# Kernel optimization log

Hardware: AMD Instinct MI355X
Metric: run time of the kernel (lower is better)

## Reference

```python
import jax, jax.numpy as jnp
import numpy as np

B, L, DIM, H = 1, 2048, 1536, 12
HD = DIM // H  # 128
SCALE = HD ** -0.5


def quantize_dequant_int8(t):
    # per-tensor symmetric int8 quantize then float dequantize (same math as torch ref)
    s = jnp.max(jnp.abs(t)) / 127.0
    q = jnp.clip(jnp.round(t / s), -128.0, 127.0)
    return q * s


def setup_inputs() -> dict:
    key = jax.random.key(0)
    ks = jax.random.split(key, 6)
    std = DIM ** -0.5
    return {
        "x": jax.random.normal(ks[0], (B, L, DIM), jnp.float32),
        "Wq": jax.random.normal(ks[1], (DIM, DIM), jnp.float32) * std,
        "Wk": jax.random.normal(ks[2], (DIM, DIM), jnp.float32) * std,
        "Wv": jax.random.normal(ks[3], (DIM, DIM), jnp.float32) * std,
        "Wo": jax.random.normal(ks[4], (DIM, DIM), jnp.float32) * std,
        "bo": jax.random.normal(ks[5], (DIM,), jnp.float32) * 0.01,
    }


def reference(x, Wq, Wk, Wv, Wo, bo):
    b, l, c = x.shape
    # QKV projections (torch Linear: x @ W^T), reshape to [B,H,L,HD]
    q = (x @ Wq.T).reshape(b, l, H, HD).transpose(0, 2, 1, 3)
    k = (x @ Wk.T).reshape(b, l, H, HD).transpose(0, 2, 1, 3)
    v = (x @ Wv.T).reshape(b, l, H, HD).transpose(0, 2, 1, 3)
    # sage-style quantize/dequant around both matmuls
    qd = quantize_dequant_int8(q)
    kd = quantize_dequant_int8(k)
    scores = jnp.einsum('bhqd,bhkd->bhqk', qd, kd) * SCALE
    probs = jax.nn.softmax(scores, axis=-1)
    pd = quantize_dequant_int8(probs)
    vd = quantize_dequant_int8(v)
    out = jnp.einsum('bhqk,bhkd->bhqd', pd, vd)  # [B,H,L,HD]
    out = out.transpose(0, 2, 1, 3).reshape(b, l, c)
    return out @ Wo.T + bo
```

## Files before the change

kernel.cpp:

```cpp
#include <hip/hip_runtime.h>
#include <stdint.h>

#define SEQ 2048
#define DIM 1536
#define NH  12
#define HD  128
#define SCALEF 0.08838834764831845f
#define LDP 40

typedef __attribute__((ext_vector_type(8))) short short8;
typedef __attribute__((ext_vector_type(4))) float floatx4;

#define MFMA16(a, b, c) __builtin_amdgcn_mfma_f32_16x16x32_bf16((a), (b), (c), 0, 0, 0)

__device__ __forceinline__ void async_cp16(const void* g, void* l) {
  __builtin_amdgcn_global_load_lds(
      (__attribute__((address_space(1))) unsigned int*)(g),
      (__attribute__((address_space(3))) unsigned int*)(l), 16, 0, 0);
}

__device__ __forceinline__ unsigned short f2bf(float f) {
  unsigned int u = __float_as_uint(f);
  u = (u + 0x7fff + ((u >> 16) & 1)) >> 16;
  return (unsigned short)u;
}

__device__ __forceinline__ void split8v(const float* x, short8& h, short8& l) {
#pragma unroll
  for (int e = 0; e < 8; e++) {
    unsigned int u = __float_as_uint(x[e]);
    h[e] = (short)(u >> 16);
    float r = x[e] - __uint_as_float(u & 0xFFFF0000u);
    l[e] = (short)f2bf(r);
  }
}
__device__ __forceinline__ void split8(const float* g, short8& h, short8& l) {
  float4 f0 = *(const float4*)g, f1 = *(const float4*)(g + 4);
  float x[8] = {f0.x, f0.y, f0.z, f0.w, f1.x, f1.y, f1.z, f1.w};
  split8v(x, h, l);
}

__global__ __launch_bounds__(256) void k_fill(float* __restrict__ out, int n,
                                              float val) {
  int i = blockIdx.x * 256 + threadIdx.x;
  if (i < n) out[i] = val;
}

__global__ __launch_bounds__(256) void k_gemm_qkv(
    const float* __restrict__ X, const float* __restrict__ Wq,
    const float* __restrict__ Wk, const float* __restrict__ Wv,
    float* __restrict__ qf, float* __restrict__ kf, float* __restrict__ vf,
    unsigned int* __restrict__ scal) {
  __shared__ __align__(16) unsigned short Ah[128 * LDP], Al[128 * LDP];
  __shared__ __align__(16) unsigned short Bh[128 * LDP], Bl[128 * LDP];
  int tid = threadIdx.x, z = blockIdx.z;
  const float* W = (z == 0) ? Wq : (z == 1) ? Wk : Wv;
  float* C = (z == 0) ? qf : (z == 1) ? kf : vf;
  int n0 = blockIdx.x * 128, m0 = blockIdx.y * 128;
  int lane = tid & 63, w = tid >> 6;
  int wr = w >> 1, wc = w & 1, lm = lane & 15, q = lane >> 4;

  floatx4 acc[4][4];
#pragma unroll
  for (int i = 0; i < 4; i++)
#pragma unroll
    for (int j = 0; j < 4; j++) acc[i][j] = (floatx4){0.f, 0.f, 0.f, 0.f};

  int rowA = tid >> 2, c8 = tid & 3;
  for (int k0 = 0; k0 < DIM; k0 += 32) {
    __syncthreads();
#pragma unroll
    for (int i = 0; i < 2; i++) {
      int r = i * 64 + rowA;
      short8 h, l;
      split8(X + (size_t)(m0 + r) * DIM + k0 + c8 * 8, h, l);
      *(short8*)(Ah + r * LDP + c8 * 8) = h;
      *(short8*)(Al + r * LDP + c8 * 8) = l;
      split8(W + (size_t)(n0 + r) * DIM + k0 + c8 * 8, h, l);
      *(short8*)(Bh + r * LDP + c8 * 8) = h;
      *(short8*)(Bl + r * LDP + c8 * 8) = l;
    }
    __syncthreads();
    short8 ah[4], al[4], bh[4], bl[4];
#pragma unroll
    for (int i = 0; i < 4; i++) {
      int r = wr * 64 + i * 16 + lm;
      ah[i] = *(const short8*)(Ah + r * LDP + q * 8);
      al[i] = *(const short8*)(Al + r * LDP + q * 8);
    }
#pragma unroll
    for (int j = 0; j < 4; j++) {
      int r = wc * 64 + j * 16 + lm;
      bh[j] = *(const short8*)(Bh + r * LDP + q * 8);
      bl[j] = *(const short8*)(Bl + r * LDP + q * 8);
    }
#pragma unroll
    for (int i = 0; i < 4; i++)
#pragma unroll
      for (int j = 0; j < 4; j++) {
        acc[i][j] = MFMA16(ah[i], bh[j], acc[i][j]);
        acc[i][j] = MFMA16(ah[i], bl[j], acc[i][j]);
        acc[i][j] = MFMA16(al[i], bh[j], acc[i][j]);
      }
  }
  float am = 0.f;
#pragma unroll
  for (int i = 0; i < 4; i++) {
    int row = m0 + wr * 64 + i * 16 + q * 4;
#pragma unroll
    for (int j = 0; j < 4; j++) {
      int col = n0 + wc * 64 + j * 16 + lm;
#pragma unroll
      for (int r = 0; r < 4; r++) {
        float v = acc[i][j][r];
        C[(size_t)(row + r) * DIM + col] = v;
        am = fmaxf(am, fabsf(v));
      }
    }
  }
#pragma unroll
  for (int mk = 32; mk >= 1; mk >>= 1) am = fmaxf(am, __shfl_xor(am, mk, 64));
  if (lane == 0) atomicMax(&scal[z], __float_as_uint(am));
}

__global__ __launch_bounds__(256) void k_quant_vT(
    const float* __restrict__ vf, const unsigned int* __restrict__ scal,
    unsigned short* __restrict__ nvT) {
  __shared__ float T[64 * 65];
  int h = blockIdx.z, d0 = blockIdx.y * 64, k0 = blockIdx.x * 64;
  float s = __uint_as_float(scal[2]) / 127.f;
  int t = threadIdx.x;
#pragma unroll
  for (int i = 0; i < 16; i++) {
    int idx = i * 256 + t;
    int r = idx >> 6, c = idx & 63;
    float v = vf[(size_t)(k0 + r) * DIM + h * HD + d0 + c];
    T[r * 65 + c] = fminf(fmaxf(rintf(v / s), -128.f), 127.f);
  }
  __syncthreads();
#pragma unroll
  for (int i = 0; i < 16; i++) {
    int idx = i * 256 + t;
    int d = idx >> 6, r = idx & 63;
    nvT[(size_t)(h * HD + d0 + d) * SEQ + k0 + r] = f2bf(T[r * 65 + d]);
  }
}

__global__ __launch_bounds__(256) void k_quant_qk(
    const float* __restrict__ qf, const float* __restrict__ kf,
    const unsigned int* __restrict__ scal,
    unsigned short* __restrict__ nq, unsigned short* __restrict__ nk) {
  int z = blockIdx.y;
  const float* src = z ? kf : qf;
  unsigned short* dst = z ? nk : nq;
  float s = __uint_as_float(scal[z]) / 127.f;
  size_t i = ((size_t)blockIdx.x * 256 + threadIdx.x) * 4;
  float4 v = *(const float4*)(src + i);
  ushort4 o;
  o.x = f2bf(fminf(fmaxf(rintf(v.x / s), -128.f), 127.f));
  o.y = f2bf(fminf(fmaxf(rintf(v.y / s), -128.f), 127.f));
  o.z = f2bf(fminf(fmaxf(rintf(v.z / s), -128.f), 127.f));
  o.w = f2bf(fminf(fmaxf(rintf(v.w / s), -128.f), 127.f));
  *(ushort4*)(dst + i) = o;
}

__global__ __launch_bounds__(256) void k_stats(
    const unsigned short* __restrict__ nq, const unsigned short* __restrict__ nk,
    const unsigned int* __restrict__ scal, float* __restrict__ pstats) {
  __shared__ unsigned short Ks[32 * 128];
  int h = blockIdx.y, tid = threadIdx.x, lane = tid & 63, w = tid >> 6;
  int lm = lane & 15, q = lane >> 4;
  int qb = blockIdx.x & 15, chunk = blockIdx.x >> 4;
  int mb = qb * 128 + w * 32;
  int kbase = chunk * 256;
  float f = (__uint_as_float(scal[0]) / 127.f) *
            (__uint_as_float(scal[1]) / 127.f) * SCALEF;

  short8 aq[2][4];
#pragma unroll
  for (int mi = 0; mi < 2; mi++) {
    const unsigned short* qb_p =
        nq + (size_t)(mb + mi * 16 + lm) * DIM + h * HD + q * 8;
#pragma unroll
    for (int cc = 0; cc < 4; cc++) aq[mi][cc] = *(const short8*)(qb_p + cc * 32);
  }

  float m[2][4], zz[2][4];
#pragma unroll
  for (int mi = 0; mi < 2; mi++)
#pragma unroll
    for (int r = 0; r < 4; r++) { m[mi][r] = -3.0e38f; zz[mi][r] = 0.f; }

  for (int kt = kbase; kt < kbase + 256; kt += 32) {
    __syncthreads();
#pragma unroll
    for (int i = 0; i < 2; i++) {
      int ch = i * 256 + tid;
      int krow = ch >> 4;
      int gcol = (ch & 15) ^ (krow & 7);
      async_cp16(nk + (size_t)(kt + krow) * DIM + h * HD + gcol * 8,
                 Ks + ch * 8);
    }
    __syncthreads();
    short8 bk[2][4];
#pragma unroll
    for (int st = 0; st < 2; st++)
#pragma unroll
      for (int cc = 0; cc < 4; cc++) {
        int phys = (cc * 4 + q) ^ (lm & 7);
        bk[st][cc] = *(const short8*)(Ks + (st * 16 + lm) * 128 + phys * 8);
      }
#pragma unroll
    for (int mi = 0; mi < 2; mi++) {
      floatx4 a0 = (floatx4){0.f, 0.f, 0.f, 0.f};
      floatx4 a1 = (floatx4){0.f, 0.f, 0.f, 0.f};
#pragma unroll
      for (int cc = 0; cc < 4; cc++) {
        a0 = MFMA16(aq[mi][cc], bk[0][cc], a0);
        a1 = MFMA16(aq[mi][cc], bk[1][cc], a1);
      }
#pragma unroll
      for (int r = 0; r < 4; r++) {
        float s0 = a0[r] * f, s1 = a1[r] * f;
        float nm = fmaxf(m[mi][r], fmaxf(s0, s1));
        zz[mi][r] = zz[mi][r] * expf(m[mi][r] - nm) + expf(s0 - nm) +
                    expf(s1 - nm);
        m[mi][r] = nm;
      }
    }
  }
#pragma unroll
  for (int mk = 1; mk < 16; mk <<= 1)
#pragma unroll
    for (int mi = 0; mi < 2; mi++)
#pragma unroll
      for (int r = 0; r < 4; r++) {
        float om = __shfl_xor(m[mi][r], mk, 64);
        float oz = __shfl_xor(zz[mi][r], mk, 64);
        float nm = fmaxf(m[mi][r], om);
        zz[mi][r] = zz[mi][r] * expf(m[mi][r] - nm) + oz * expf(om - nm);
        m[mi][r] = nm;
      }
  if (lm == 0) {
#pragma unroll
    for (int mi = 0; mi < 2; mi++)
#pragma unroll
      for (int r = 0; r < 4; r++) {
        int row = mb + mi * 16 + q * 4 + r;
        float* p = pstats + (((size_t)h * SEQ + row) * 8 + chunk) * 2;
        p[0] = m[mi][r];
        p[1] = zz[mi][r];
      }
  }
}

__global__ __launch_bounds__(256) void k_merge(
    const float* __restrict__ pstats, float* __restrict__ stats,
    unsigned int* __restrict__ minZ) {
  int idx = blockIdx.x * 256 + threadIdx.x;
  const float* p = pstats + (size_t)idx * 16;
  float M = -3.0e38f;
#pragma unroll
  for (int c = 0; c < 8; c++) M = fmaxf(M, p[c * 2]);
  float Z = 0.f;
#pragma unroll
  for (int c = 0; c < 8; c++) Z += p[c * 2 + 1] * expf(p[c * 2] - M);
  stats[(size_t)idx * 2] = M;
  stats[(size_t)idx * 2 + 1] = Z;
  atomicMin(minZ, __float_as_uint(Z));
}

__global__ __launch_bounds__(256) void k_attn(
    const unsigned short* __restrict__ nq, const unsigned short* __restrict__ nk,
    const unsigned short* __restrict__ nvT,
    const unsigned int* __restrict__ scal, const unsigned int* __restrict__ minZ,
    const float* __restrict__ stats, float* __restrict__ attn0,
    float* __restrict__ attn1) {
  __shared__ unsigned short Ks[32 * 128];
  __shared__ unsigned short Vs[128 * 32];
  __shared__ unsigned short Pl[4][2][16 * 40];
  int h = blockIdx.y, tid = threadIdx.x, lane = tid & 63, w = tid >> 6;
  int lm = lane & 15, q = lane >> 4;
  int qb = blockIdx.x & 15, chunk = blockIdx.x >> 4;
  int mb = qb * 128 + w * 32;
  float* attn = chunk ? attn1 : attn0;
  float sv = __uint_as_float(scal[2]) / 127.f;
  float f = (__uint_as_float(scal[0]) / 127.f) *
            (__uint_as_float(scal[1]) / 127.f) * SCALEF;
  float sp = (1.f / __uint_as_float(*minZ)) / 127.f;
  float inv_sp = 1.f / sp;

  short8 aq[2][4];
#pragma unroll
  for (int mi = 0; mi < 2; mi++) {
    const unsigned short* qb_p =
        nq + (size_t)(mb + mi * 16 + lm) * DIM + h * HD + q * 8;
#pragma unroll
    for (int cc = 0; cc < 4; cc++) aq[mi][cc] = *(const short8*)(qb_p + cc * 32);
  }
  float M[2][4], invZ[2][4];
#pragma unroll
  for (int mi = 0; mi < 2; mi++)
#pragma unroll
    for (int r = 0; r < 4; r++) {
      int row = mb + mi * 16 + q * 4 + r;
      M[mi][r] = stats[((size_t)h * SEQ + row) * 2];
      invZ[mi][r] = 1.f / stats[((size_t)h * SEQ + row) * 2 + 1];
    }
  floatx4 accO[2][8];
#pragma unroll
  for (int mi = 0; mi < 2; mi++)
#pragma unroll
    for (int j = 0; j < 8; j++) accO[mi][j] = (floatx4){0.f, 0.f, 0.f, 0.f};

  int kbase = chunk * 1024;
  for (int kt = kbase; kt < kbase + 1024; kt += 32) {
    __syncthreads();
#pragma unroll
    for (int i = 0; i < 2; i++) {
      int ch = i * 256 + tid;
      int krow = ch >> 4;
      int gcol = (ch & 15) ^ (krow & 7);
      async_cp16(nk + (size_t)(kt + krow) * DIM + h * HD + gcol * 8,
                 Ks + ch * 8);
      int d = ch >> 2;
      int vcol = (ch & 3) ^ ((d >> 1) & 3);
      async_cp16(nvT + (size_t)(h * HD + d) * SEQ + kt + vcol * 8,
                 Vs + ch * 8);
    }
    __syncthreads();
    short8 bk[2][4];
#pragma unroll
    for (int st = 0; st < 2; st++)
#pragma unroll
      for (int cc = 0; cc < 4; cc++) {
        int phys = (cc * 4 + q) ^ (lm & 7);
        bk[st][cc] = *(const short8*)(Ks + (st * 16 + lm) * 128 + phys * 8);
      }
#pragma unroll
    for (int mi = 0; mi < 2; mi++)
#pragma unroll
      for (int st = 0; st < 2; st++) {
        floatx4 acc = (floatx4){0.f, 0.f, 0.f, 0.f};
#pragma unroll
        for (int cc = 0; cc < 4; cc++) acc = MFMA16(aq[mi][cc], bk[st][cc], acc);
#pragma unroll
        for (int r = 0; r < 4; r++) {
          float t = expf(acc[r] * f - M[mi][r]);
          float n = rintf(t * invZ[mi][r] * inv_sp);
          n = fminf(n, 127.f);
          Pl[w][mi][(q * 4 + r) * 40 + st * 16 + lm] = f2bf(n);
        }
      }
    __syncthreads();
    short8 ap[2];
#pragma unroll
    for (int mi = 0; mi < 2; mi++)
      ap[mi] = *(const short8*)(&Pl[w][mi][lm * 40 + q * 8]);
#pragma unroll
    for (int j = 0; j < 8; j++) {
      int d = j * 16 + lm;
      int vphys = q ^ ((d >> 1) & 3);
      short8 bv = *(const short8*)(Vs + d * 32 + vphys * 8);
#pragma unroll
      for (int mi = 0; mi < 2; mi++) accO[mi][j] = MFMA16(ap[mi], bv, accO[mi][j]);
    }
  }
  float osc = sp * sv;
#pragma unroll
  for (int mi = 0; mi < 2; mi++)
#pragma unroll
    for (int j = 0; j < 8; j++)
#pragma unroll
      for (int r = 0; r < 4; r++)
        attn[(size_t)(mb + mi * 16 + q * 4 + r) * DIM + h * HD + j * 16 + lm] =
            accO[mi][j][r] * osc;
}

__global__ __launch_bounds__(256) void k_gemm_out(
    const float* __restrict__ A0, const float* __restrict__ A1,
    const float* __restrict__ Wo, const float* __restrict__ bo,
    float* __restrict__ out) {
  __shared__ __align__(16) unsigned short Ah[128 * LDP], Al[128 * LDP];
  __shared__ __align__(16) unsigned short Bh[128 * LDP], Bl[128 * LDP];
  int tid = threadIdx.x;
  int n0 = blockIdx.x * 128, m0 = blockIdx.y * 128;
  int lane = tid & 63, w = tid >> 6;
  int wr = w >> 1, wc = w & 1, lm = lane & 15, q = lane >> 4;

  floatx4 acc[4][4];
#pragma unroll
  for (int i = 0; i < 4; i++)
#pragma unroll
    for (int j = 0; j < 4; j++) acc[i][j] = (floatx4){0.f, 0.f, 0.f, 0.f};

  int rowA = tid >> 2, c8 = tid & 3;
  for (int k0 = 0; k0 < DIM; k0 += 32) {
    __syncthreads();
#pragma unroll
    for (int i = 0; i < 2; i++) {
      int r = i * 64 + rowA;
      size_t off = (size_t)(m0 + r) * DIM + k0 + c8 * 8;
      float4 x0 = *(const float4*)(A0 + off), x1 = *(const float4*)(A0 + off + 4);
      float4 y0 = *(const float4*)(A1 + off), y1 = *(const float4*)(A1 + off + 4);
      float xs[8] = {x0.x + y0.x, x0.y + y0.y, x0.z + y0.z, x0.w + y0.w,
                     x1.x + y1.x, x1.y + y1.y, x1.z + y1.z, x1.w + y1.w};
      short8 h, l;
      split8v(xs, h, l);
      *(short8*)(Ah + r * LDP + c8 * 8) = h;
      *(short8*)(Al + r * LDP + c8 * 8) = l;
      split8(Wo + (size_t)(n0 + r) * DIM + k0 + c8 * 8, h, l);
      *(short8*)(Bh + r * LDP + c8 * 8) = h;
      *(short8*)(Bl + r * LDP + c8 * 8) = l;
    }
    __syncthreads();
    short8 ah[4], al[4], bh[4], bl[4];
#pragma unroll
    for (int i = 0; i < 4; i++) {
      int r = wr * 64 + i * 16 + lm;
      ah[i] = *(const short8*)(Ah + r * LDP + q * 8);
      al[i] = *(const short8*)(Al + r * LDP + q * 8);
    }
#pragma unroll
    for (int j = 0; j < 4; j++) {
      int r = wc * 64 + j * 16 + lm;
      bh[j] = *(const short8*)(Bh + r * LDP + q * 8);
      bl[j] = *(const short8*)(Bl + r * LDP + q * 8);
    }
#pragma unroll
    for (int i = 0; i < 4; i++)
#pragma unroll
      for (int j = 0; j < 4; j++) {
        acc[i][j] = MFMA16(ah[i], bh[j], acc[i][j]);
        acc[i][j] = MFMA16(ah[i], bl[j], acc[i][j]);
        acc[i][j] = MFMA16(al[i], bh[j], acc[i][j]);
      }
  }
#pragma unroll
  for (int j = 0; j < 4; j++) {
    int col = n0 + wc * 64 + j * 16 + lm;
    float bias = bo[col];
#pragma unroll
    for (int i = 0; i < 4; i++) {
      int row = m0 + wr * 64 + i * 16 + q * 4;
#pragma unroll
      for (int r = 0; r < 4; r++)
        out[(size_t)(row + r) * DIM + col] = acc[i][j][r] + bias;
    }
  }
}

extern "C" void kernel_launch(void* const* d_in, const int* in_sizes, int n_in,
                              void* d_out, int out_size, void* d_ws, size_t ws_size,
                              hipStream_t stream) {
  float* out = (float*)d_out;
  bool sizes_ok = (n_in >= 6) && in_sizes && in_sizes[0] == SEQ * DIM &&
                  in_sizes[1] == DIM * DIM && in_sizes[2] == DIM * DIM &&
                  in_sizes[3] == DIM * DIM && in_sizes[4] == DIM * DIM &&
                  in_sizes[5] == DIM && out_size == SEQ * DIM;
  if (!sizes_ok) {
    k_fill<<<(out_size + 255) / 256, 256, 0, stream>>>(out, out_size, 1.0f);
    return;
  }
  if (ws_size < 50528272) {
    k_fill<<<(out_size + 255) / 256, 256, 0, stream>>>(out, out_size, 2.0f);
    return;
  }

  const float* x  = (const float*)d_in[0];
  const float* Wq = (const float*)d_in[1];
  const float* Wk = (const float*)d_in[2];
  const float* Wv = (const float*)d_in[3];
  const float* Wo = (const float*)d_in[4];
  const float* bo = (const float*)d_in[5];
  char* ws = (char*)d_ws;

  float* qf = (float*)(ws);
  float* kf = (float*)(ws + 12582912);
  float* vf = (float*)(ws + 25165824);
  unsigned short* nq  = (unsigned short*)(ws + 25165824);
  float* pstats = (float*)(ws + 31457280);
  unsigned short* nvT = (unsigned short*)(ws + 37748736);
  unsigned short* nk  = (unsigned short*)(ws + 44040192);
  float* attn0 = qf;
  float* attn1 = kf;
  float* stats = (float*)(ws + 50331648);
  unsigned int* scal = (unsigned int*)(ws + 50528256);

  hipMemsetAsync(scal, 0, 12, stream);
  hipMemsetAsync(scal + 3, 0x7f, 4, stream);

  k_gemm_qkv<<<dim3(DIM / 128, SEQ / 128, 3), 256, 0, stream>>>(
      x, Wq, Wk, Wv, qf, kf, vf, scal);
  k_quant_vT<<<dim3(SEQ / 64, HD / 64, NH), 256, 0, stream>>>(vf, scal, nvT);
  k_quant_qk<<<dim3((SEQ * DIM) / 1024, 2), 256, 0, stream>>>(qf, kf, scal, nq, nk);
  k_stats<<<dim3(8 * 16, NH), 256, 0, stream>>>(nq, nk, scal, pstats);
  k_merge<<<dim3(NH * SEQ / 256), 256, 0, stream>>>(pstats, stats, scal + 3);
  k_attn<<<dim3(2 * 16, NH), 256, 0, stream>>>(nq, nk, nvT, scal, scal + 3,
                                               stats, attn0, attn1);
  k_gemm_out<<<dim3(DIM / 128, SEQ / 128), 256, 0, stream>>>(attn0, attn1, Wo,
                                                             bo, out);
}
```

Before: 531.7 us.

## Double-buffer LDS tiles with register prefetch in QKV and output GEMMs

The QKV and output projection GEMMs now use two LDS buffers. The next K-slice's global loads are issued into registers before the current slice's MFMAs, then split into bf16 hi/lo and stored into the other buffer afterwards. This hides global-load latency behind compute and removes one of the two barriers per iteration. In exchange it doubles LDS use per block (about 80KB), which may lower occupancy, and adds register pressure from the prefetched float4 values.

```diff
diff --git a/kernel.cpp b/kernel.cpp
--- a/kernel.cpp
+++ b/kernel.cpp
@@ -51,8 +51,8 @@
     const float* __restrict__ Wk, const float* __restrict__ Wv,
     float* __restrict__ qf, float* __restrict__ kf, float* __restrict__ vf,
     unsigned int* __restrict__ scal) {
-  __shared__ __align__(16) unsigned short Ah[128 * LDP], Al[128 * LDP];
-  __shared__ __align__(16) unsigned short Bh[128 * LDP], Bl[128 * LDP];
+  __shared__ __align__(16) unsigned short Ah[2][128 * LDP], Al[2][128 * LDP];
+  __shared__ __align__(16) unsigned short Bh[2][128 * LDP], Bl[2][128 * LDP];
   int tid = threadIdx.x, z = blockIdx.z;
   const float* W = (z == 0) ? Wq : (z == 1) ? Wk : Wv;
   float* C = (z == 0) ? qf : (z == 1) ? kf : vf;
@@ -67,32 +67,59 @@
     for (int j = 0; j < 4; j++) acc[i][j] = (floatx4){0.f, 0.f, 0.f, 0.f};
 
   int rowA = tid >> 2, c8 = tid & 3;
-  for (int k0 = 0; k0 < DIM; k0 += 32) {
-    __syncthreads();
-#pragma unroll
-    for (int i = 0; i < 2; i++) {
-      int r = i * 64 + rowA;
-      short8 h, l;
-      split8(X + (size_t)(m0 + r) * DIM + k0 + c8 * 8, h, l);
-      *(short8*)(Ah + r * LDP + c8 * 8) = h;
-      *(short8*)(Al + r * LDP + c8 * 8) = l;
-      split8(W + (size_t)(n0 + r) * DIM + k0 + c8 * 8, h, l);
-      *(short8*)(Bh + r * LDP + c8 * 8) = h;
-      *(short8*)(Bl + r * LDP + c8 * 8) = l;
-    }
-    __syncthreads();
+  const float* pA0 = X + (size_t)(m0 + rowA) * DIM + c8 * 8;
+  const float* pA1 = pA0 + (size_t)64 * DIM;
+  const float* pB0 = W + (size_t)(n0 + rowA) * DIM + c8 * 8;
+  const float* pB1 = pB0 + (size_t)64 * DIM;
+
+  {
+    short8 h, l;
+    split8(pA0, h, l);
+    *(short8*)(&Ah[0][0] + rowA * LDP + c8 * 8) = h;
+    *(short8*)(&Al[0][0] + rowA * LDP + c8 * 8) = l;
+    split8(pA1, h, l);
+    *(short8*)(&Ah[0][0] + (64 + rowA) * LDP + c8 * 8) = h;
+    *(short8*)(&Al[0][0] + (64 + rowA) * LDP + c8 * 8) = l;
+    split8(pB0, h, l);
+    *(short8*)(&Bh[0][0] + rowA * LDP + c8 * 8) = h;
+    *(short8*)(&Bl[0][0] + rowA * LDP + c8 * 8) = l;
+    split8(pB1, h, l);
+    *(short8*)(&Bh[0][0] + (64 + rowA) * LDP + c8 * 8) = h;
+    *(short8*)(&Bl[0][0] + (64 + rowA) * LDP + c8 * 8) = l;
+  }
+  __syncthreads();
+
+  int cur = 0;
+  for (int it = 0; it < DIM / 32; ++it) {
+    int kn = it * 32 + 32;
+    bool more = kn < DIM;
+    float4 a00, a01, a10, a11, b00, b01, b10, b11;
+    if (more) {
+      a00 = *(const float4*)(pA0 + kn);
+      a01 = *(const float4*)(pA0 + kn + 4);
+      a10 = *(const float4*)(pA1 + kn);
+      a11 = *(const float4*)(pA1 + kn + 4);
+      b00 = *(const float4*)(pB0 + kn);
+      b01 = *(const float4*)(pB0 + kn + 4);
+      b10 = *(const float4*)(pB1 + kn);
+      b11 = *(const float4*)(pB1 + kn + 4);
+    }
+    const unsigned short* AhC = &Ah[cur][0];
+    const unsigned short* AlC = &Al[cur][0];
+    const unsigned short* BhC = &Bh[cur][0];
+    const unsigned short* BlC = &Bl[cur][0];
     short8 ah[4], al[4], bh[4], bl[4];
 #pragma unroll
     for (int i = 0; i < 4; i++) {
       int r = wr * 64 + i * 16 + lm;
-      ah[i] = *(const short8*)(Ah + r * LDP + q * 8);
-      al[i] = *(const short8*)(Al + r * LDP + q * 8);
+      ah[i] = *(const short8*)(AhC + r * LDP + q * 8);
+      al[i] = *(const short8*)(AlC + r * LDP + q * 8);
     }
 #pragma unroll
     for (int j = 0; j < 4; j++) {
       int r = wc * 64 + j * 16 + lm;
-      bh[j] = *(const short8*)(Bh + r * LDP + q * 8);
-      bl[j] = *(const short8*)(Bl + r * LDP + q * 8);
+      bh[j] = *(const short8*)(BhC + r * LDP + q * 8);
+      bl[j] = *(const short8*)(BlC + r * LDP + q * 8);
     }
 #pragma unroll
     for (int i = 0; i < 4; i++)
@@ -102,6 +129,39 @@
         acc[i][j] = MFMA16(ah[i], bl[j], acc[i][j]);
         acc[i][j] = MFMA16(al[i], bh[j], acc[i][j]);
       }
+    if (more) {
+      unsigned short* AhN = &Ah[cur ^ 1][0];
+      unsigned short* AlN = &Al[cur ^ 1][0];
+      unsigned short* BhN = &Bh[cur ^ 1][0];
+      unsigned short* BlN = &Bl[cur ^ 1][0];
+      short8 h, l;
+      {
+        float xs[8] = {a00.x, a00.y, a00.z, a00.w, a01.x, a01.y, a01.z, a01.w};
+        split8v(xs, h, l);
+        *(short8*)(AhN + rowA * LDP + c8 * 8) = h;
+        *(short8*)(AlN + rowA * LDP + c8 * 8) = l;
+      }
+      {
+        float xs[8] = {a10.x, a10.y, a10.z, a10.w, a11.x, a11.y, a11.z, a11.w};
+        split8v(xs, h, l);
+        *(short8*)(AhN + (64 + rowA) * LDP + c8 * 8) = h;
+        *(short8*)(AlN + (64 + rowA) * LDP + c8 * 8) = l;
+      }
+      {
+        float xs[8] = {b00.x, b00.y, b00.z, b00.w, b01.x, b01.y, b01.z, b01.w};
+        split8v(xs, h, l);
+        *(short8*)(BhN + rowA * LDP + c8 * 8) = h;
+        *(short8*)(BlN + rowA * LDP + c8 * 8) = l;
+      }
+      {
+        float xs[8] = {b10.x, b10.y, b10.z, b10.w, b11.x, b11.y, b11.z, b11.w};
+        split8v(xs, h, l);
+        *(short8*)(BhN + (64 + rowA) * LDP + c8 * 8) = h;
+        *(short8*)(BlN + (64 + rowA) * LDP + c8 * 8) = l;
+      }
+      __syncthreads();
+    }
+    cur ^= 1;
   }
   float am = 0.f;
 #pragma unroll
@@ -381,8 +441,8 @@
     const float* __restrict__ A0, const float* __restrict__ A1,
     const float* __restrict__ Wo, const float* __restrict__ bo,
     float* __restrict__ out) {
-  __shared__ __align__(16) unsigned short Ah[128 * LDP], Al[128 * LDP];
-  __shared__ __align__(16) unsigned short Bh[128 * LDP], Bl[128 * LDP];
+  __shared__ __align__(16) unsigned short Ah[2][128 * LDP], Al[2][128 * LDP];
+  __shared__ __align__(16) unsigned short Bh[2][128 * LDP], Bl[2][128 * LDP];
   int tid = threadIdx.x;
   int n0 = blockIdx.x * 128, m0 = blockIdx.y * 128;
   int lane = tid & 63, w = tid >> 6;
@@ -395,37 +455,75 @@
     for (int j = 0; j < 4; j++) acc[i][j] = (floatx4){0.f, 0.f, 0.f, 0.f};
 
   int rowA = tid >> 2, c8 = tid & 3;
-  for (int k0 = 0; k0 < DIM; k0 += 32) {
-    __syncthreads();
-#pragma unroll
-    for (int i = 0; i < 2; i++) {
-      int r = i * 64 + rowA;
-      size_t off = (size_t)(m0 + r) * DIM + k0 + c8 * 8;
-      float4 x0 = *(const float4*)(A0 + off), x1 = *(const float4*)(A0 + off + 4);
-      float4 y0 = *(const float4*)(A1 + off), y1 = *(const float4*)(A1 + off + 4);
+  size_t offA0 = (size_t)(m0 + rowA) * DIM + c8 * 8;
+  size_t offA1 = offA0 + (size_t)64 * DIM;
+  const float* pB0 = Wo + (size_t)(n0 + rowA) * DIM + c8 * 8;
+  const float* pB1 = pB0 + (size_t)64 * DIM;
+
+  {
+    short8 h, l;
+    {
+      float4 x0 = *(const float4*)(A0 + offA0), x1 = *(const float4*)(A0 + offA0 + 4);
+      float4 y0 = *(const float4*)(A1 + offA0), y1 = *(const float4*)(A1 + offA0 + 4);
       float xs[8] = {x0.x + y0.x, x0.y + y0.y, x0.z + y0.z, x0.w + y0.w,
                      x1.x + y1.x, x1.y + y1.y, x1.z + y1.z, x1.w + y1.w};
-      short8 h, l;
       split8v(xs, h, l);
-      *(short8*)(Ah + r * LDP + c8 * 8) = h;
-      *(short8*)(Al + r * LDP + c8 * 8) = l;
-      split8(Wo + (size_t)(n0 + r) * DIM + k0 + c8 * 8, h, l);
-      *(short8*)(Bh + r * LDP + c8 * 8) = h;
-      *(short8*)(Bl + r * LDP + c8 * 8) = l;
-    }
-    __syncthreads();
+      *(short8*)(&Ah[0][0] + rowA * LDP + c8 * 8) = h;
+      *(short8*)(&Al[0][0] + rowA * LDP + c8 * 8) = l;
+    }
+    {
+      float4 x0 = *(const float4*)(A0 + offA1), x1 = *(const float4*)(A0 + offA1 + 4);
+      float4 y0 = *(const float4*)(A1 + offA1), y1 = *(const float4*)(A1 + offA1 + 4);
+      float xs[8] = {x0.x + y0.x, x0.y + y0.y, x0.z + y0.z, x0.w + y0.w,
+                     x1.x + y1.x, x1.y + y1.y, x1.z + y1.z, x1.w + y1.w};
+      split8v(xs, h, l);
+      *(short8*)(&Ah[0][0] + (64 + rowA) * LDP + c8 * 8) = h;
+      *(short8*)(&Al[0][0] + (64 + rowA) * LDP + c8 * 8) = l;
+    }
+    split8(pB0, h, l);
+    *(short8*)(&Bh[0][0] + rowA * LDP + c8 * 8) = h;
+    *(short8*)(&Bl[0][0] + rowA * LDP + c8 * 8) = l;
+    split8(pB1, h, l);
+    *(short8*)(&Bh[0][0] + (64 + rowA) * LDP + c8 * 8) = h;
+    *(short8*)(&Bl[0][0] + (64 + rowA) * LDP + c8 * 8) = l;
+  }
+  __syncthreads();
+
+  int cur = 0;
+  for (int it = 0; it < DIM / 32; ++it) {
+    int kn = it * 32 + 32;
+    bool more = kn < DIM;
+    float4 x00, x01, x10, x11, y00, y01, y10, y11, b00, b01, b10, b11;
+    if (more) {
+      x00 = *(const float4*)(A0 + offA0 + kn);
+      x01 = *(const float4*)(A0 + offA0 + kn + 4);
+      y00 = *(const float4*)(A1 + offA0 + kn);
+      y01 = *(const float4*)(A1 + offA0 + kn + 4);
+      x10 = *(const float4*)(A0 + offA1 + kn);
+      x11 = *(const float4*)(A0 + offA1 + kn + 4);
+      y10 = *(const float4*)(A1 + offA1 + kn);
+      y11 = *(const float4*)(A1 + offA1 + kn + 4);
+      b00 = *(const float4*)(pB0 + kn);
+      b01 = *(const float4*)(pB0 + kn + 4);
+      b10 = *(const float4*)(pB1 + kn);
+      b11 = *(const float4*)(pB1 + kn + 4);
+    }
+    const unsigned short* AhC = &Ah[cur][0];
+    const unsigned short* AlC = &Al[cur][0];
+    const unsigned short* BhC = &Bh[cur][0];
+    const unsigned short* BlC = &Bl[cur][0];
     short8 ah[4], al[4], bh[4], bl[4];
 #pragma unroll
     for (int i = 0; i < 4; i++) {
       int r = wr * 64 + i * 16 + lm;
-      ah[i] = *(const short8*)(Ah + r * LDP + q * 8);
-      al[i] = *(const short8*)(Al + r * LDP + q * 8);
+      ah[i] = *(const short8*)(AhC + r * LDP + q * 8);
+      al[i] = *(const short8*)(AlC + r * LDP + q * 8);
     }
 #pragma unroll
     for (int j = 0; j < 4; j++) {
       int r = wc * 64 + j * 16 + lm;
-      bh[j] = *(const short8*)(Bh + r * LDP + q * 8);
-      bl[j] = *(const short8*)(Bl + r * LDP + q * 8);
+      bh[j] = *(const short8*)(BhC + r * LDP + q * 8);
+      bl[j] = *(const short8*)(BlC + r * LDP + q * 8);
     }
 #pragma unroll
     for (int i = 0; i < 4; i++)
@@ -435,6 +533,41 @@
         acc[i][j] = MFMA16(ah[i], bl[j], acc[i][j]);
         acc[i][j] = MFMA16(al[i], bh[j], acc[i][j]);
       }
+    if (more) {
+      unsigned short* AhN = &Ah[cur ^ 1][0];
+      unsigned short* AlN = &Al[cur ^ 1][0];
+      unsigned short* BhN = &Bh[cur ^ 1][0];
+      unsigned short* BlN = &Bl[cur ^ 1][0];
+      short8 h, l;
+      {
+        float xs[8] = {x00.x + y00.x, x00.y + y00.y, x00.z + y00.z, x00.w + y00.w,
+                       x01.x + y01.x, x01.y + y01.y, x01.z + y01.z, x01.w + y01.w};
+        split8v(xs, h, l);
+        *(short8*)(AhN + rowA * LDP + c8 * 8) = h;
+        *(short8*)(AlN + rowA * LDP + c8 * 8) = l;
+      }
+      {
+        float xs[8] = {x10.x + y10.x, x10.y + y10.y, x10.z + y10.z, x10.w + y10.w,
+                       x11.x + y11.x, x11.y + y11.y, x11.z + y11.z, x11.w + y11.w};
+        split8v(xs, h, l);
+        *(short8*)(AhN + (64 + rowA) * LDP + c8 * 8) = h;
+        *(short8*)(AlN + (64 + rowA) * LDP + c8 * 8) = l;
+      }
+      {
+        float xs[8] = {b00.x, b00.y, b00.z, b00.w, b01.x, b01.y, b01.z, b01.w};
+        split8v(xs, h, l);
+        *(short8*)(BhN + rowA * LDP + c8 * 8) = h;
+        *(short8*)(BlN + rowA * LDP + c8 * 8) = l;
+      }
+      {
+        float xs[8] = {b10.x, b10.y, b10.z, b10.w, b11.x, b11.y, b11.z, b11.w};
+        split8v(xs, h, l);
+        *(short8*)(BhN + (64 + rowA) * LDP + c8 * 8) = h;
+        *(short8*)(BlN + (64 + rowA) * LDP + c8 * 8) = l;
+      }
+      __syncthreads();
+    }
+    cur ^= 1;
   }
 #pragma unroll
   for (int j = 0; j < 4; j++) {
```

Measured after the change: 536.8 us. About the same (+1.0%).

## Presplit GEMM activations to bf16 hi/lo and double-buffer tiles with async LDS loads

Applied to the files above, without the earlier changes.

Adds pre-pass kernels that split X and the summed attention output into bf16 high/low arrays once, instead of redoing the split inside every GEMM block. The QKV and output GEMMs now load A tiles straight into LDS with async global-to-LDS copies into a swizzled layout. Both LDS buffers are double-buffered so the next K-slice (async A, register-prefetched and split W) loads while the current one is in MFMAs, with one barrier per iteration. The cost is two extra kernel launches and extra global traffic for the split arrays, plus doubled shared memory per block, which can reduce occupancy.

```diff
diff --git a/kernel.cpp b/kernel.cpp
--- a/kernel.cpp
+++ b/kernel.cpp
@@ -46,13 +46,38 @@
   if (i < n) out[i] = val;
 }
 
+__global__ __launch_bounds__(256) void k_split_x(
+    const float* __restrict__ X, unsigned short* __restrict__ Xh,
+    unsigned short* __restrict__ Xl) {
+  size_t i = ((size_t)blockIdx.x * 256 + threadIdx.x) * 8;
+  short8 h, l;
+  split8(X + i, h, l);
+  *(short8*)(Xh + i) = h;
+  *(short8*)(Xl + i) = l;
+}
+
+__global__ __launch_bounds__(256) void k_split_o(
+    const float* __restrict__ A0, const float* __restrict__ A1,
+    unsigned short* __restrict__ Oh, unsigned short* __restrict__ Ol) {
+  size_t i = ((size_t)blockIdx.x * 256 + threadIdx.x) * 8;
+  float4 x0 = *(const float4*)(A0 + i), x1 = *(const float4*)(A0 + i + 4);
+  float4 y0 = *(const float4*)(A1 + i), y1 = *(const float4*)(A1 + i + 4);
+  float xs[8] = {x0.x + y0.x, x0.y + y0.y, x0.z + y0.z, x0.w + y0.w,
+                 x1.x + y1.x, x1.y + y1.y, x1.z + y1.z, x1.w + y1.w};
+  short8 h, l;
+  split8v(xs, h, l);
+  *(short8*)(Oh + i) = h;
+  *(short8*)(Ol + i) = l;
+}
+
 __global__ __launch_bounds__(256) void k_gemm_qkv(
-    const float* __restrict__ X, const float* __restrict__ Wq,
-    const float* __restrict__ Wk, const float* __restrict__ Wv,
-    float* __restrict__ qf, float* __restrict__ kf, float* __restrict__ vf,
+    const unsigned short* __restrict__ Xh, const unsigned short* __restrict__ Xl,
+    const float* __restrict__ Wq, const float* __restrict__ Wk,
+    const float* __restrict__ Wv, float* __restrict__ qf,
+    float* __restrict__ kf, float* __restrict__ vf,
     unsigned int* __restrict__ scal) {
-  __shared__ __align__(16) unsigned short Ah[128 * LDP], Al[128 * LDP];
-  __shared__ __align__(16) unsigned short Bh[128 * LDP], Bl[128 * LDP];
+  __shared__ __align__(16) unsigned short Ahs[2][128 * 32], Als[2][128 * 32];
+  __shared__ __align__(16) unsigned short Bh[2][128 * LDP], Bl[2][128 * LDP];
   int tid = threadIdx.x, z = blockIdx.z;
   const float* W = (z == 0) ? Wq : (z == 1) ? Wk : Wv;
   float* C = (z == 0) ? qf : (z == 1) ? kf : vf;
@@ -67,32 +92,93 @@
     for (int j = 0; j < 4; j++) acc[i][j] = (floatx4){0.f, 0.f, 0.f, 0.f};
 
   int rowA = tid >> 2, c8 = tid & 3;
-  for (int k0 = 0; k0 < DIM; k0 += 32) {
-    __syncthreads();
-#pragma unroll
-    for (int i = 0; i < 2; i++) {
-      int r = i * 64 + rowA;
-      short8 h, l;
-      split8(X + (size_t)(m0 + r) * DIM + k0 + c8 * 8, h, l);
-      *(short8*)(Ah + r * LDP + c8 * 8) = h;
-      *(short8*)(Al + r * LDP + c8 * 8) = l;
-      split8(W + (size_t)(n0 + r) * DIM + k0 + c8 * 8, h, l);
-      *(short8*)(Bh + r * LDP + c8 * 8) = h;
-      *(short8*)(Bl + r * LDP + c8 * 8) = l;
-    }
-    __syncthreads();
+  const float* pB0 = W + (size_t)(n0 + rowA) * DIM + c8 * 8;
+  const float* pB1 = pB0 + (size_t)64 * DIM;
+  int sidx0 = tid, sidx1 = 256 + tid;
+  int smr0 = sidx0 >> 2, sq0 = (sidx0 & 3) ^ ((smr0 >> 1) & 3);
+  int smr1 = sidx1 >> 2, sq1 = (sidx1 & 3) ^ ((smr1 >> 1) & 3);
+  size_t gofA0 = (size_t)(m0 + smr0) * DIM + sq0 * 8;
+  size_t gofA1 = (size_t)(m0 + smr1) * DIM + sq1 * 8;
+  int phA = (q ^ ((lm >> 1) & 3)) * 8;
+  int mrbase = wr * 64 + lm;
+
+  {
+    async_cp16(Xh + gofA0, &Ahs[0][0] + sidx0 * 8);
+    async_cp16(Xl + gofA0, &Als[0][0] + sidx0 * 8);
+    async_cp16(Xh + gofA1, &Ahs[0][0] + sidx1 * 8);
+    async_cp16(Xl + gofA1, &Als[0][0] + sidx1 * 8);
+    short8 h, l;
+    split8(pB0, h, l);
+    *(short8*)(&Bh[0][0] + rowA * LDP + c8 * 8) = h;
+    *(short8*)(&Bl[0][0] + rowA * LDP + c8 * 8) = l;
+    split8(pB1, h, l);
+    *(short8*)(&Bh[0][0] + (64 + rowA) * LDP + c8 * 8) = h;
+    *(short8*)(&Bl[0][0] + (64 + rowA) * LDP + c8 * 8) = l;
+  }
+  __syncthreads();
+
+  for (int it = 0; it < 47; ++it) {
+    int cur = it & 1, nxt = cur ^ 1;
+    int kn = it * 32 + 32;
+    float4 b00 = *(const float4*)(pB0 + kn);
+    float4 b01 = *(const float4*)(pB0 + kn + 4);
+    float4 b10 = *(const float4*)(pB1 + kn);
+    float4 b11 = *(const float4*)(pB1 + kn + 4);
+    async_cp16(Xh + gofA0 + kn, &Ahs[nxt][0] + sidx0 * 8);
+    async_cp16(Xl + gofA0 + kn, &Als[nxt][0] + sidx0 * 8);
+    async_cp16(Xh + gofA1 + kn, &Ahs[nxt][0] + sidx1 * 8);
+    async_cp16(Xl + gofA1 + kn, &Als[nxt][0] + sidx1 * 8);
     short8 ah[4], al[4], bh[4], bl[4];
 #pragma unroll
     for (int i = 0; i < 4; i++) {
-      int r = wr * 64 + i * 16 + lm;
-      ah[i] = *(const short8*)(Ah + r * LDP + q * 8);
-      al[i] = *(const short8*)(Al + r * LDP + q * 8);
+      int off = (mrbase + i * 16) * 32 + phA;
+      ah[i] = *(const short8*)(&Ahs[cur][0] + off);
+      al[i] = *(const short8*)(&Als[cur][0] + off);
     }
 #pragma unroll
     for (int j = 0; j < 4; j++) {
       int r = wc * 64 + j * 16 + lm;
-      bh[j] = *(const short8*)(Bh + r * LDP + q * 8);
-      bl[j] = *(const short8*)(Bl + r * LDP + q * 8);
+      bh[j] = *(const short8*)(&Bh[cur][0] + r * LDP + q * 8);
+      bl[j] = *(const short8*)(&Bl[cur][0] + r * LDP + q * 8);
+    }
+#pragma unroll
+    for (int i = 0; i < 4; i++)
+#pragma unroll
+      for (int j = 0; j < 4; j++) {
+        acc[i][j] = MFMA16(ah[i], bh[j], acc[i][j]);
+        acc[i][j] = MFMA16(ah[i], bl[j], acc[i][j]);
+        acc[i][j] = MFMA16(al[i], bh[j], acc[i][j]);
+      }
+    {
+      short8 h, l;
+      {
+        float xs[8] = {b00.x, b00.y, b00.z, b00.w, b01.x, b01.y, b01.z, b01.w};
+        split8v(xs, h, l);
+        *(short8*)(&Bh[nxt][0] + rowA * LDP + c8 * 8) = h;
+        *(short8*)(&Bl[nxt][0] + rowA * LDP + c8 * 8) = l;
+      }
+      {
+        float xs[8] = {b10.x, b10.y, b10.z, b10.w, b11.x, b11.y, b11.z, b11.w};
+        split8v(xs, h, l);
+        *(short8*)(&Bh[nxt][0] + (64 + rowA) * LDP + c8 * 8) = h;
+        *(short8*)(&Bl[nxt][0] + (64 + rowA) * LDP + c8 * 8) = l;
+      }
+    }
+    __syncthreads();
+  }
+  {
+    short8 ah[4], al[4], bh[4], bl[4];
+#pragma unroll
+    for (int i = 0; i < 4; i++) {
+      int off = (mrbase + i * 16) * 32 + phA;
+      ah[i] = *(const short8*)(&Ahs[1][0] + off);
+      al[i] = *(const short8*)(&Als[1][0] + off);
+    }
+#pragma unroll
+    for (int j = 0; j < 4; j++) {
+      int r = wc * 64 + j * 16 + lm;
+      bh[j] = *(const short8*)(&Bh[1][0] + r * LDP + q * 8);
+      bl[j] = *(const short8*)(&Bl[1][0] + r * LDP + q * 8);
     }
 #pragma unroll
     for (int i = 0; i < 4; i++)
@@ -378,11 +464,11 @@
 }
 
 __global__ __launch_bounds__(256) void k_gemm_out(
-    const float* __restrict__ A0, const float* __restrict__ A1,
+    const unsigned short* __restrict__ Oh, const unsigned short* __restrict__ Ol,
     const float* __restrict__ Wo, const float* __restrict__ bo,
     float* __restrict__ out) {
-  __shared__ __align__(16) unsigned short Ah[128 * LDP], Al[128 * LDP];
-  __shared__ __align__(16) unsigned short Bh[128 * LDP], Bl[128 * LDP];
+  __shared__ __align__(16) unsigned short Ahs[2][128 * 32], Als[2][128 * 32];
+  __shared__ __align__(16) unsigned short Bh[2][128 * LDP], Bl[2][128 * LDP];
   int tid = threadIdx.x;
   int n0 = blockIdx.x * 128, m0 = blockIdx.y * 128;
   int lane = tid & 63, w = tid >> 6;
@@ -395,37 +481,93 @@
     for (int j = 0; j < 4; j++) acc[i][j] = (floatx4){0.f, 0.f, 0.f, 0.f};
 
   int rowA = tid >> 2, c8 = tid & 3;
-  for (int k0 = 0; k0 < DIM; k0 += 32) {
-    __syncthreads();
-#pragma unroll
-    for (int i = 0; i < 2; i++) {
-      int r = i * 64 + rowA;
-      size_t off = (size_t)(m0 + r) * DIM + k0 + c8 * 8;
-      float4 x0 = *(const float4*)(A0 + off), x1 = *(const float4*)(A0 + off + 4);
-      float4 y0 = *(const float4*)(A1 + off), y1 = *(const float4*)(A1 + off + 4);
-      float xs[8] = {x0.x + y0.x, x0.y + y0.y, x0.z + y0.z, x0.w + y0.w,
-                     x1.x + y1.x, x1.y + y1.y, x1.z + y1.z, x1.w + y1.w};
-      short8 h, l;
-      split8v(xs, h, l);
-      *(short8*)(Ah + r * LDP + c8 * 8) = h;
-      *(short8*)(Al + r * LDP + c8 * 8) = l;
-      split8(Wo + (size_t)(n0 + r) * DIM + k0 + c8 * 8, h, l);
-      *(short8*)(Bh + r * LDP + c8 * 8) = h;
-      *(short8*)(Bl + r * LDP + c8 * 8) = l;
-    }
-    __syncthreads();
+  const float* pB0 = Wo + (size_t)(n0 + rowA) * DIM + c8 * 8;
+  const float* pB1 = pB0 + (size_t)64 * DIM;
+  int sidx0 = tid, sidx1 = 256 + tid;
+  int smr0 = sidx0 >> 2, sq0 = (sidx0 & 3) ^ ((smr0 >> 1) & 3);
+  int smr1 = sidx1 >> 2, sq1 = (sidx1 & 3) ^ ((smr1 >> 1) & 3);
+  size_t gofA0 = (size_t)(m0 + smr0) * DIM + sq0 * 8;
+  size_t gofA1 = (size_t)(m0 + smr1) * DIM + sq1 * 8;
+  int phA = (q ^ ((lm >> 1) & 3)) * 8;
+  int mrbase = wr * 64 + lm;
+
+  {
+    async_cp16(Oh + gofA0, &Ahs[0][0] + sidx0 * 8);
+    async_cp16(Ol + gofA0, &Als[0][0] + sidx0 * 8);
+    async_cp16(Oh + gofA1, &Ahs[0][0] + sidx1 * 8);
+    async_cp16(Ol + gofA1, &Als[0][0] + sidx1 * 8);
+    short8 h, l;
+    split8(pB0, h, l);
+    *(short8*)(&Bh[0][0] + rowA * LDP + c8 * 8) = h;
+    *(short8*)(&Bl[0][0] + rowA * LDP + c8 * 8) = l;
+    split8(pB1, h, l);
+    *(short8*)(&Bh[0][0] + (64 + rowA) * LDP + c8 * 8) = h;
+    *(short8*)(&Bl[0][0] + (64 + rowA) * LDP + c8 * 8) = l;
+  }
+  __syncthreads();
+
+  for (int it = 0; it < 47; ++it) {
+    int cur = it & 1, nxt = cur ^ 1;
+    int kn = it * 32 + 32;
+    float4 b00 = *(const float4*)(pB0 + kn);
+    float4 b01 = *(const float4*)(pB0 + kn + 4);
+    float4 b10 = *(const float4*)(pB1 + kn);
+    float4 b11 = *(const float4*)(pB1 + kn + 4);
+    async_cp16(Oh + gofA0 + kn, &Ahs[nxt][0] + sidx0 * 8);
+    async_cp16(Ol + gofA0 + kn, &Als[nxt][0] + sidx0 * 8);
+    async_cp16(Oh + gofA1 + kn, &Ahs[nxt][0] + sidx1 * 8);
+    async_cp16(Ol + gofA1 + kn, &Als[nxt][0] + sidx1 * 8);
     short8 ah[4], al[4], bh[4], bl[4];
 #pragma unroll
     for (int i = 0; i < 4; i++) {
-      int r = wr * 64 + i * 16 + lm;
-      ah[i] = *(const short8*)(Ah + r * LDP + q * 8);
-      al[i] = *(const short8*)(Al + r * LDP + q * 8);
+      int off = (mrbase + i * 16) * 32 + phA;
+      ah[i] = *(const short8*)(&Ahs[cur][0] + off);
+      al[i] = *(const short8*)(&Als[cur][0] + off);
     }
 #pragma unroll
     for (int j = 0; j < 4; j++) {
       int r = wc * 64 + j * 16 + lm;
-      bh[j] = *(const short8*)(Bh + r * LDP + q * 8);
-      bl[j] = *(const short8*)(Bl + r * LDP + q * 8);
+      bh[j] = *(const short8*)(&Bh[cur][0] + r * LDP + q * 8);
+      bl[j] = *(const short8*)(&Bl[cur][0] + r * LDP + q * 8);
+    }
+#pragma unroll
+    for (int i = 0; i < 4; i++)
+#pragma unroll
+      for (int j = 0; j < 4; j++) {
+        acc[i][j] = MFMA16(ah[i], bh[j], acc[i][j]);
+        acc[i][j] = MFMA16(ah[i], bl[j], acc[i][j]);
+        acc[i][j] = MFMA16(al[i], bh[j], acc[i][j]);
+      }
+    {
+      short8 h, l;
+      {
+        float xs[8] = {b00.x, b00.y, b00.z, b00.w, b01.x, b01.y, b01.z, b01.w};
+        split8v(xs, h, l);
+        *(short8*)(&Bh[nxt][0] + rowA * LDP + c8 * 8) = h;
+        *(short8*)(&Bl[nxt][0] + rowA * LDP + c8 * 8) = l;
+      }
+      {
+        float xs[8] = {b10.x, b10.y, b10.z, b10.w, b11.x, b11.y, b11.z, b11.w};
+        split8v(xs, h, l);
+        *(short8*)(&Bh[nxt][0] + (64 + rowA) * LDP + c8 * 8) = h;
+        *(short8*)(&Bl[nxt][0] + (64 + rowA) * LDP + c8 * 8) = l;
+      }
+    }
+    __syncthreads();
+  }
+  {
+    short8 ah[4], al[4], bh[4], bl[4];
+#pragma unroll
+    for (int i = 0; i < 4; i++) {
+      int off = (mrbase + i * 16) * 32 + phA;
+      ah[i] = *(const short8*)(&Ahs[1][0] + off);
+      al[i] = *(const short8*)(&Als[1][0] + off);
+    }
+#pragma unroll
+    for (int j = 0; j < 4; j++) {
+      int r = wc * 64 + j * 16 + lm;
+      bh[j] = *(const short8*)(&Bh[1][0] + r * LDP + q * 8);
+      bl[j] = *(const short8*)(&Bl[1][0] + r * LDP + q * 8);
     }
 #pragma unroll
     for (int i = 0; i < 4; i++)
@@ -482,6 +624,10 @@
   float* pstats = (float*)(ws + 31457280);
   unsigned short* nvT = (unsigned short*)(ws + 37748736);
   unsigned short* nk  = (unsigned short*)(ws + 44040192);
+  unsigned short* Xh = nvT;
+  unsigned short* Xl = nk;
+  unsigned short* Oh = nvT;
+  unsigned short* Ol = nk;
   float* attn0 = qf;
   float* attn1 = kf;
   float* stats = (float*)(ws + 50331648);
@@ -490,14 +636,15 @@
   hipMemsetAsync(scal, 0, 12, stream);
   hipMemsetAsync(scal + 3, 0x7f, 4, stream);
 
+  k_split_x<<<dim3(SEQ * DIM / 2048), 256, 0, stream>>>(x, Xh, Xl);
   k_gemm_qkv<<<dim3(DIM / 128, SEQ / 128, 3), 256, 0, stream>>>(
-      x, Wq, Wk, Wv, qf, kf, vf, scal);
+      Xh, Xl, Wq, Wk, Wv, qf, kf, vf, scal);
   k_quant_vT<<<dim3(SEQ / 64, HD / 64, NH), 256, 0, stream>>>(vf, scal, nvT);
   k_quant_qk<<<dim3((SEQ * DIM) / 1024, 2), 256, 0, stream>>>(qf, kf, scal, nq, nk);
   k_stats<<<dim3(8 * 16, NH), 256, 0, stream>>>(nq, nk, scal, pstats);
   k_merge<<<dim3(NH * SEQ / 256), 256, 0, stream>>>(pstats, stats, scal + 3);
   k_attn<<<dim3(2 * 16, NH), 256, 0, stream>>>(nq, nk, nvT, scal, scal + 3,
                                                stats, attn0, attn1);
-  k_gemm_out<<<dim3(DIM / 128, SEQ / 128), 256, 0, stream>>>(attn0, attn1, Wo,
-                                                             bo, out);
-}
+  k_split_o<<<dim3(SEQ * DIM / 2048), 256, 0, stream>>>(attn0, attn1, Oh, Ol);
+  k_gemm_out<<<dim3(DIM / 128, SEQ / 128), 256, 0, stream>>>(Oh, Ol, Wo, bo, out);
+}
```

Result: no change. 525.5 us (-1.2%).
